# Performance work log

Hardware: AMD Instinct MI355X
Metric: run time of the kernel (lower is better)

Reference implementation:

```python
import jax, jax.numpy as jnp
import numpy as np
from jax import lax

N, M, T, IN, H, DEPTH = 64, 10, 160, 40, 256, 3
B = N * M
EPS = 1e-8


def setup_inputs() -> dict:
    key = jax.random.key(0)
    ks = jax.random.split(key, 20)
    s = 1.0 / np.sqrt(H)  # torch LSTM init scale
    inp = {
        "sequences": jax.random.normal(ks[0], (B, T, IN), jnp.float32),
        "len_sequences": jax.random.randint(ks[1], (B,), 80, T + 1, jnp.int32),
        "w_sim": jnp.float32(0.5),
        "b_sim": jnp.float32(0.5),
    }
    in_sizes = [IN, H, H]
    for l in range(DEPTH):
        k = 2 + 4 * l
        inp[f"Wih{l}"] = jax.random.uniform(ks[k], (4 * H, in_sizes[l]), jnp.float32, -s, s)
        inp[f"Whh{l}"] = jax.random.uniform(ks[k + 1], (4 * H, H), jnp.float32, -s, s)
        inp[f"bih{l}"] = jax.random.uniform(ks[k + 2], (4 * H,), jnp.float32, -s, s)
        inp[f"bhh{l}"] = jax.random.uniform(ks[k + 3], (4 * H,), jnp.float32, -s, s)
    return inp


def _lstm_layer(x_tbf, mask_tb, Wih, Whh, bih, bhh):
    """x_tbf: [T,B,F] time-major. mask_tb: [T,B] valid-step mask.
    Returns (h_seq [T,B,H], c_last [B,H]) where c_last is the cell state at
    the last valid timestep of each sequence (packed-sequence semantics)."""
    b = x_tbf.shape[1]
    h0 = jnp.zeros((b, H), x_tbf.dtype)
    c0 = jnp.zeros((b, H), x_tbf.dtype)

    def step(carry, xm):
        h, c = carry
        xt, mt = xm
        g = xt @ Wih.T + bih + h @ Whh.T + bhh  # [B,4H]
        i, f, gg, o = jnp.split(g, 4, axis=1)
        cn = jax.nn.sigmoid(f) * c + jax.nn.sigmoid(i) * jnp.tanh(gg)
        hn = jax.nn.sigmoid(o) * jnp.tanh(cn)
        m = mt[:, None]
        h2 = jnp.where(m, hn, h)
        c2 = jnp.where(m, cn, c)
        return (h2, c2), h2

    (hT, cT), h_seq = lax.scan(step, (h0, c0), (x_tbf, mask_tb))
    return h_seq, cT


def reference(sequences, len_sequences, Wih0, Whh0, bih0, bhh0,
              Wih1, Whh1, bih1, bhh1, Wih2, Whh2, bih2, bhh2,
              w_sim, b_sim):
    lens = len_sequences.astype(jnp.int32)
    x = jnp.transpose(sequences, (1, 0, 2))  # [T,B,IN]
    mask = jnp.arange(T)[:, None] < lens[None, :]  # [T,B]

    layers = [(Wih0, Whh0, bih0, bhh0), (Wih1, Whh1, bih1, bhh1), (Wih2, Whh2, bih2, bhh2)]
    c_last = None
    for (Wih, Whh, bih, bhh) in layers:
        x, c_last = _lstm_layer(x, mask, Wih, Whh, bih, bhh)
    E = c_last  # [B,H] final-layer cell state per utterance (original order)

    # L2-normalize embeddings (F.normalize, p=2, dim=1)
    E = E / jnp.maximum(jnp.linalg.norm(E, axis=1, keepdims=True), 1e-12)

    Er = E.reshape(N, M, H)
    C = Er.mean(axis=1)  # [N,H] speaker centroids
    # exclusive centroids exactly as source: (M*c_j + E_i)/(M-1)
    Cm = ((M * C[:, None, :] + Er) / (M - 1)).reshape(B, H)

    En = E / jnp.maximum(jnp.linalg.norm(E, axis=1, keepdims=True), EPS)
    Cn = C / jnp.maximum(jnp.linalg.norm(C, axis=1, keepdims=True), EPS)
    Cmn = Cm / jnp.maximum(jnp.linalg.norm(Cm, axis=1, keepdims=True), EPS)

    S = (En @ Cn.T) * w_sim + b_sim  # [B,N]: cos(E_i, c_j)*w + b

    # diagonal block: row i, col i//M uses exclusive centroid
    d = jnp.sum(En * Cmn, axis=1)  # [B]
    rows = jnp.arange(B)
    cols = jnp.repeat(jnp.arange(N), M)
    S = S.at[rows, cols].set(d * w_sim + b_sim)
    return S


if __name__ == "__main__":
    out = reference(**setup_inputs())
    print(out.shape, out.dtype)
```

## Files before the change

kernel.cpp:

```cpp
#include <hip/hip_runtime.h>
#include <cstdint>
#include <cstddef>

typedef __attribute__((ext_vector_type(8))) short short8;
typedef __attribute__((ext_vector_type(4))) float f32x4;
typedef __attribute__((ext_vector_type(4))) unsigned short us4;

#define N_SPK 64
#define M_UTT 10
#define T_SEQ 160
#define IN_F  40
#define H_DIM 256
#define B_TOT 640
#define G4    1024
#define FSTR  64

__device__ __forceinline__ unsigned short f2bf(float f) {
  unsigned int u = __float_as_uint(f);
  u += 0x7FFFu + ((u >> 16) & 1u);
  return (unsigned short)(u >> 16);
}
__device__ __forceinline__ float b2f(unsigned short u) {
  return __uint_as_float(((unsigned int)u) << 16);
}
__device__ __forceinline__ float sigm(float x) {
  return 1.f / (1.f + __expf(-x));
}
__device__ __forceinline__ float tanh_fast(float x) {
  return 1.f - 2.f / (1.f + __expf(2.f * x));
}
__device__ __forceinline__ unsigned long long ato_ld(const unsigned long long* p) {
  return __hip_atomic_load(p, __ATOMIC_RELAXED, __HIP_MEMORY_SCOPE_AGENT);
}
__device__ __forceinline__ void ato_st(unsigned long long* p, unsigned long long v) {
  __hip_atomic_store(p, v, __ATOMIC_RELAXED, __HIP_MEMORY_SCOPE_AGENT);
}
__device__ __forceinline__ int flg_ld(const int* p) {
  return __hip_atomic_load(p, __ATOMIC_RELAXED, __HIP_MEMORY_SCOPE_AGENT);
}
__device__ __forceinline__ void flg_st(int* p, int v) {
  __hip_atomic_store(p, v, __ATOMIC_RELAXED, __HIP_MEMORY_SCOPE_AGENT);
}

__global__ void pack_w_kernel(const float* __restrict__ W, short* __restrict__ out,
                              int Kin, int Ktiles) {
  int idx = blockIdx.x * 256 + threadIdx.x;
  int total = 64 * Ktiles * 64;
  if (idx >= total) return;
  int lane = idx & 63;
  int rest = idx >> 6;
  int ks   = rest % Ktiles;
  int tile = rest / Ktiles;
  int n  = tile * 16 + (lane & 15);
  int k0 = ks * 32 + (lane >> 4) * 8;
  short8 v;
#pragma unroll
  for (int j = 0; j < 8; ++j) {
    int k = k0 + j;
    float f = (k < Kin) ? W[(size_t)n * Kin + k] : 0.f;
    v[j] = (short)f2bf(f);
  }
  *(short8*)&out[(size_t)idx * 8] = v;
}

__global__ void bias_sum_kernel(const float* __restrict__ a, const float* __restrict__ b,
                                float* __restrict__ o) {
  int i = blockIdx.x * 256 + threadIdx.x;
  if (i < G4) o[i] = a[i] + b[i];
}

__global__ __launch_bounds__(256, 2)
void gate_gemm0(const float* __restrict__ seq, const short* __restrict__ Wp,
                const float* __restrict__ bias, unsigned short* __restrict__ G) {
  const int btile = blockIdx.x % 40;
  const int rest  = blockIdx.x / 40;
  const int tg    = rest & 3;
  const int chunk = rest >> 2;
  const int tid = threadIdx.x, lane = tid & 63, wave = tid >> 6;
  const int nl = lane & 15, mq = lane >> 4;

  for (int mg = 0; mg < 4; ++mg) {
    const int t0 = chunk * 16 + mg * 4;
    f32x4 acc[4][4];
#pragma unroll
    for (int q = 0; q < 4; ++q) {
      int tile = tg * 16 + wave + 4 * q;
      float bv = bias[tile * 16 + nl];
#pragma unroll
      for (int mm = 0; mm < 4; ++mm) acc[mm][q] = (f32x4){bv, bv, bv, bv};
    }
    for (int kt = 0; kt < 2; ++kt) {
      short8 a[4];
      const int m = btile * 16 + nl;
      const int k0 = kt * 32 + mq * 8;
#pragma unroll
      for (int mm = 0; mm < 4; ++mm) {
#pragma unroll
        for (int j = 0; j < 8; ++j) {
          int k = k0 + j;
          float f = (k < IN_F) ? seq[((size_t)m * T_SEQ + (t0 + mm)) * IN_F + k] : 0.f;
          a[mm][j] = (short)f2bf(f);
        }
      }
#pragma unroll
      for (int q = 0; q < 4; ++q) {
        int tile = tg * 16 + wave + 4 * q;
        short8 b = *(const short8*)&Wp[(((size_t)tile * 2 + kt) * 64 + lane) * 8];
#pragma unroll
        for (int mm = 0; mm < 4; ++mm)
          acc[mm][q] = __builtin_amdgcn_mfma_f32_16x16x32_bf16(a[mm], b, acc[mm][q], 0, 0, 0);
      }
    }
#pragma unroll
    for (int mm = 0; mm < 4; ++mm)
#pragma unroll
      for (int q = 0; q < 4; ++q) {
        int tile = tg * 16 + wave + 4 * q;
        us4 o;
#pragma unroll
        for (int r = 0; r < 4; ++r) o[r] = f2bf(acc[mm][q][r]);
        *(us4*)&G[(((size_t)(t0 + mm) * 40 + btile) * 64 + tile) * 256 + lane * 4] = o;
      }
  }
}

template<int L>
__device__ __forceinline__ void rec_stage(
    int S, int hb,
    const short* __restrict__ Whhp, const short* __restrict__ Wihp,
    const unsigned short* __restrict__ G0, const float* __restrict__ biasl,
    unsigned long long* __restrict__ hxch, int* __restrict__ flags,
    const int* __restrict__ lens, float* __restrict__ c_state,
    unsigned short* h_sh, unsigned short* x_sh, float* c_sh,
    float* bias_sh, short* wih_lds, int* len_sh)
{
  const int tid = threadIdx.x, lane = tid & 63, wave = tid >> 6;
  const int mq = lane >> 4, nl = lane & 15;
  const int lc = wave * 16 + nl;
  const int colown = hb * 64 + lc;
  unsigned long long* x64 = (unsigned long long*)x_sh;

  short8 wregH[4][8];
#pragma unroll
  for (int g = 0; g < 4; ++g) {
    const int tile = g * 16 + hb * 4 + wave;
#pragma unroll
    for (int kt = 0; kt < 8; ++kt)
      wregH[g][kt] = *(const short8*)&Whhp[(((size_t)tile * 8 + kt) * 64 + lane) * 8];
  }
  short8 wregI[4][4];
  if (L >= 1) {
#pragma unroll
    for (int g = 0; g < 4; ++g) {
      const int tile = g * 16 + hb * 4 + wave;
#pragma unroll
      for (int kt = 0; kt < 4; ++kt)
        wregI[g][kt] = *(const short8*)&Wihp[(((size_t)tile * 8 + kt) * 64 + lane) * 8];
    }
    for (int i = tid; i < 4096; i += 256) {
      int tl = i >> 6, ln = i & 63;
      int lt = tl >> 2, kt4 = tl & 3;
      int gt = (lt >> 2) * 16 + hb * 4 + (lt & 3);
      *(short8*)&wih_lds[(lt * 4 + kt4) * 512 + ln * 8] =
          *(const short8*)&Wihp[(((size_t)gt * 8 + 4 + kt4) * 64 + ln) * 8];
    }
    for (int i = tid; i < 1024; i += 256) bias_sh[i] = biasl[i];
  }
  for (int i = tid; i < 64 * 264; i += 256) h_sh[i] = 0;
  for (int i = tid; i < 64 * 65; i += 256) c_sh[i] = 0.f;
  if (tid < 64) len_sh[tid] = lens[S * 64 + tid];

  if (L == 0) {
    us4 tmp[16];
#pragma unroll
    for (int m = 0; m < 4; ++m)
#pragma unroll
      for (int g = 0; g < 4; ++g) {
        const int tile = g * 16 + hb * 4 + wave;
        tmp[m * 4 + g] = *(const us4*)&G0[(((size_t)0 * 40 + S * 4 + m) * 64 + tile) * 256 + lane * 4];
      }
#pragma unroll
    for (int u = 0; u < 16; ++u)
      x64[u * 256 + tid] = *(unsigned long long*)&tmp[u];
  }
  __syncthreads();

  const int fself = L * 40 + S * 4 + hb;

  for (int t = 0; t < T_SEQ; ++t) {
    const int par = t & 3;
    if (L >= 1 && tid < 4)
      while (flg_ld(&flags[((L - 1) * 40 + S * 4 + tid) * FSTR]) < t + 1) {}
    if (L < 2 && tid >= 4 && tid < 8)
      while (flg_ld(&flags[((L + 1) * 40 + S * 4 + (tid - 4)) * FSTR]) < t - 3) {}
    __syncthreads();

    unsigned long long xr[16];
    if (L >= 1) {
      const unsigned long long* xb =
          hxch + ((size_t)((par * 3 + (L - 1)) * 10 + S)) * 4096;
#pragma unroll
      for (int u = 0; u < 16; ++u) xr[u] = ato_ld(&xb[u * 256 + tid]);
    }
    f32x4 acc[4][4];
    if (L == 0) {
#pragma unroll
      for (int m = 0; m < 4; ++m)
#pragma unroll
        for (int g = 0; g < 4; ++g) {
          unsigned long long v = x64[(m * 4 + g) * 256 + tid];
          us4 gv = *(us4*)&v;
#pragma unroll
          for (int r = 0; r < 4; ++r) acc[m][g][r] = b2f(gv[r]);
        }
    } else {
#pragma unroll
      for (int g = 0; g < 4; ++g) {
        const int tile = g * 16 + hb * 4 + wave;
        float bv = bias_sh[tile * 16 + nl];
#pragma unroll
        for (int m = 0; m < 4; ++m) acc[m][g] = (f32x4){bv, bv, bv, bv};
      }
    }
#pragma unroll
    for (int kt = 0; kt < 8; ++kt) {
      short8 a[4];
#pragma unroll
      for (int m = 0; m < 4; ++m)
        a[m] = *(const short8*)&h_sh[(m * 16 + nl) * 264 + kt * 32 + mq * 8];
#pragma unroll
      for (int m = 0; m < 4; ++m)
#pragma unroll
        for (int g = 0; g < 4; ++g)
          acc[m][g] = __builtin_amdgcn_mfma_f32_16x16x32_bf16(a[m], wregH[g][kt], acc[m][g], 0, 0, 0);
    }
    if (L >= 1) {
#pragma unroll
      for (int u = 0; u < 16; ++u) {
        int j = u * 256 + tid, pp = j >> 10, jj = j & 1023;
        *(unsigned long long*)&x_sh[(jj >> 4) * 264 + pp * 64 + (jj & 15) * 4] = xr[u];
      }
      __syncthreads();
#pragma unroll
      for (int kt = 0; kt < 8; ++kt) {
        short8 a[4];
#pragma unroll
        for (int m = 0; m < 4; ++m)
          a[m] = *(const short8*)&x_sh[(m * 16 + nl) * 264 + kt * 32 + mq * 8];
#pragma unroll
        for (int g = 0; g < 4; ++g) {
          short8 b = (kt < 4) ? wregI[g][kt]
                              : *(const short8*)&wih_lds[((g * 4 + wave) * 4 + (kt - 4)) * 512 + lane * 8];
#pragma unroll
          for (int m = 0; m < 4; ++m)
            acc[m][g] = __builtin_amdgcn_mfma_f32_16x16x32_bf16(a[m], b, acc[m][g], 0, 0, 0);
        }
      }
    }
    unsigned short hv[16];
#pragma unroll
    for (int m = 0; m < 4; ++m)
#pragma unroll
      for (int r = 0; r < 4; ++r) {
        const int row = m * 16 + mq * 4 + r;
        float c_old = c_sh[row * 65 + lc];
        float cn = sigm(acc[m][1][r]) * c_old + sigm(acc[m][0][r]) * tanh_fast(acc[m][2][r]);
        float hn = sigm(acc[m][3][r]) * tanh_fast(cn);
        bool upd = t < len_sh[row];
        if (upd) c_sh[row * 65 + lc] = cn;
        hv[m * 4 + r] = upd ? f2bf(hn) : h_sh[row * 264 + colown];
      }
    __syncthreads();
#pragma unroll
    for (int m = 0; m < 4; ++m)
#pragma unroll
      for (int r = 0; r < 4; ++r)
        h_sh[(m * 16 + mq * 4 + r) * 264 + colown] = hv[m * 4 + r];
    __syncthreads();
    unsigned long long* myslab =
        hxch + ((size_t)((par * 3 + L) * 10 + S) * 4 + hb) * 1024;
    for (int j = tid; j < 1024; j += 256) {
      int sample = j >> 4, l4 = j & 15;
      unsigned long long v =
          *(const unsigned long long*)&h_sh[sample * 264 + hb * 64 + l4 * 4];
      ato_st(&myslab[j], v);
    }
    __syncthreads();
    if (tid == 0) flg_st(&flags[fself * FSTR], t + 1);
    if (L == 0) {
      int tn = (t + 1 < T_SEQ) ? t + 1 : t;
      us4 tmp[16];
#pragma unroll
      for (int m = 0; m < 4; ++m)
#pragma unroll
        for (int g = 0; g < 4; ++g) {
          const int tile = g * 16 + hb * 4 + wave;
          tmp[m * 4 + g] = *(const us4*)&G0[(((size_t)tn * 40 + S * 4 + m) * 64 + tile) * 256 + lane * 4];
        }
#pragma unroll
      for (int u = 0; u < 16; ++u)
        x64[u * 256 + tid] = *(unsigned long long*)&tmp[u];
    }
    if (tid < 3) {
      int p = tid + (tid >= hb ? 1 : 0);
      while (flg_ld(&flags[(L * 40 + S * 4 + p) * FSTR]) < t + 1) {}
    }
    __syncthreads();
    {
      unsigned long long pr[12];
#pragma unroll
      for (int u = 0; u < 12; ++u) {
        int j = u * 256 + tid;
        int pp = j >> 10, jj = j & 1023;
        int p = pp + (pp >= hb ? 1 : 0);
        pr[u] = ato_ld(&hxch[((size_t)((par * 3 + L) * 10 + S) * 4 + p) * 1024 + jj]);
      }
#pragma unroll
      for (int u = 0; u < 12; ++u) {
        int j = u * 256 + tid;
        int pp = j >> 10, jj = j & 1023;
        int p = pp + (pp >= hb ? 1 : 0);
        *(unsigned long long*)&h_sh[(jj >> 4) * 264 + p * 64 + (jj & 15) * 4] = pr[u];
      }
    }
    __syncthreads();
  }
  if (L == 2) {
#pragma unroll
    for (int m = 0; m < 4; ++m)
#pragma unroll
      for (int r = 0; r < 4; ++r) {
        const int row = m * 16 + mq * 4 + r;
        c_state[((size_t)S * 64 + row) * 256 + colown] = c_sh[row * 65 + lc];
      }
  }
}

__global__ __launch_bounds__(256, 1)
void fused_lstm(const short* __restrict__ Whhp_all, const short* __restrict__ Wih1p,
                const short* __restrict__ Wih2p, const float* __restrict__ biasc,
                const unsigned short* __restrict__ G0, const int* __restrict__ lens,
                unsigned long long* __restrict__ hxch, int* __restrict__ flags,
                float* __restrict__ c_state)
{
  __shared__ unsigned short h_sh[64 * 264];
  __shared__ unsigned short x_sh[64 * 264];
  __shared__ float c_sh[64 * 65];
  __shared__ float bias_sh[1024];
  __shared__ short wih_lds[16 * 4 * 512];
  __shared__ int len_sh[64];

  const int bid  = blockIdx.x;
  const int xcd  = bid & 7;
  const int j    = bid >> 3;
  const int g    = (j >> 2) * 8 + xcd;
  if (g >= 30) return;
  const int L  = g / 10;
  const int S  = g % 10;
  const int hb = j & 3;

  if (L == 0)
    rec_stage<0>(S, hb, Whhp_all,          nullptr, G0, nullptr,
                 hxch, flags, lens, c_state, h_sh, x_sh, c_sh, bias_sh, wih_lds, len_sh);
  else if (L == 1)
    rec_stage<1>(S, hb, Whhp_all + 262144, Wih1p, G0, biasc + G4,
                 hxch, flags, lens, c_state, h_sh, x_sh, c_sh, bias_sh, wih_lds, len_sh);
  else
    rec_stage<2>(S, hb, Whhp_all + 524288, Wih2p, G0, biasc + 2 * G4,
                 hxch, flags, lens, c_state, h_sh, x_sh, c_sh, bias_sh, wih_lds, len_sh);
}

__global__ void k_norm(const float* __restrict__ E, float* __restrict__ E1,
                       float* __restrict__ En) {
  int row  = blockIdx.x * 4 + (threadIdx.x >> 6);
  int lane = threadIdx.x & 63;
  const float* e = E + (size_t)row * H_DIM;
  float v[4]; float ss = 0.f;
#pragma unroll
  for (int j = 0; j < 4; ++j) { v[j] = e[lane + 64 * j]; ss += v[j] * v[j]; }
#pragma unroll
  for (int m = 32; m >= 1; m >>= 1) ss += __shfl_xor(ss, m, 64);
  float nrm  = sqrtf(ss);
  float inv1 = 1.f / fmaxf(nrm, 1e-12f);
  float inv2 = 1.f / fmaxf(nrm * inv1, 1e-8f);
#pragma unroll
  for (int j = 0; j < 4; ++j) {
    float e1 = v[j] * inv1;
    E1[(size_t)row * H_DIM + lane + 64 * j] = e1;
    En[(size_t)row * H_DIM + lane + 64 * j] = e1 * inv2;
  }
}

__global__ void k_cent(const float* __restrict__ E1, float* __restrict__ C,
                       float* __restrict__ CnT) {
  int n = blockIdx.x;
  int lane = threadIdx.x;
  float v[4]; float ss = 0.f;
#pragma unroll
  for (int j = 0; j < 4; ++j) {
    int col = lane + 64 * j;
    float s = 0.f;
    for (int m = 0; m < M_UTT; ++m) s += E1[((size_t)n * M_UTT + m) * H_DIM + col];
    v[j] = s / (float)M_UTT;
    ss += v[j] * v[j];
  }
#pragma unroll
  for (int m = 32; m >= 1; m >>= 1) ss += __shfl_xor(ss, m, 64);
  float inv = 1.f / fmaxf(sqrtf(ss), 1e-8f);
#pragma unroll
  for (int j = 0; j < 4; ++j) {
    int col = lane + 64 * j;
    C[(size_t)n * H_DIM + col]  = v[j];
    CnT[(size_t)col * N_SPK + n] = v[j] * inv;
  }
}

__global__ void k_cm(const float* __restrict__ E1, const float* __restrict__ C,
                     float* __restrict__ Cmn) {
  int b    = blockIdx.x * 4 + (threadIdx.x >> 6);
  int lane = threadIdx.x & 63;
  int spk  = b / M_UTT;
  float v[4]; float ss = 0.f;
#pragma unroll
  for (int j = 0; j < 4; ++j) {
    int col = lane + 64 * j;
    v[j] = ((float)M_UTT * C[(size_t)spk * H_DIM + col] + E1[(size_t)b * H_DIM + col])
           / (float)(M_UTT - 1);
    ss += v[j] * v[j];
  }
#pragma unroll
  for (int m = 32; m >= 1; m >>= 1) ss += __shfl_xor(ss, m, 64);
  float inv = 1.f / fmaxf(sqrtf(ss), 1e-8f);
#pragma unroll
  for (int j = 0; j < 4; ++j)
    Cmn[(size_t)b * H_DIM + lane + 64 * j] = v[j] * inv;
}

__global__ void k_sim(const float* __restrict__ En, const float* __restrict__ CnT,
                      const float* __restrict__ Cmn, const float* __restrict__ w_sim,
                      const float* __restrict__ b_sim, float* __restrict__ S) {
  int b = blockIdx.x;
  int n = threadIdx.x;
  int diag = b / M_UTT;
  float w = w_sim[0], bb = b_sim[0];
  float s = 0.f;
  for (int k = 0; k < H_DIM; ++k) {
    float en = En[(size_t)b * H_DIM + k];
    float c  = (n == diag) ? Cmn[(size_t)b * H_DIM + k] : CnT[(size_t)k * N_SPK + n];
    s += en * c;
  }
  S[(size_t)b * N_SPK + n] = s * w + bb;
}

#define O_WHH   0ull
#define O_WIH0  1572864ull
#define O_WIH1  1703936ull
#define O_WIH2  2228224ull
#define O_BIAS  2752512ull
#define O_CST   2764800ull
#define O_E1    3420160ull
#define O_EN    4075520ull
#define O_C     4730880ull
#define O_CNT   4796416ull
#define O_CMN   4861952ull
#define O_FLG   5517312ull
#define O_HXCH  5548032ull
#define O_G0    9480192ull

extern "C" void kernel_launch(void* const* d_in, const int* in_sizes, int n_in,
                              void* d_out, int out_size, void* d_ws, size_t ws_size,
                              hipStream_t stream) {
  const float* seq   = (const float*)d_in[0];
  const int*   lens  = (const int*)d_in[1];
  const float* w_sim = (const float*)d_in[2];
  const float* b_sim = (const float*)d_in[3];
  const float* Wih[3] = {(const float*)d_in[4],  (const float*)d_in[8],  (const float*)d_in[12]};
  const float* Whh[3] = {(const float*)d_in[5],  (const float*)d_in[9],  (const float*)d_in[13]};
  const float* bih[3] = {(const float*)d_in[6],  (const float*)d_in[10], (const float*)d_in[14]};
  const float* bhh[3] = {(const float*)d_in[7],  (const float*)d_in[11], (const float*)d_in[15]};

  char* ws = (char*)d_ws;
  short* Whhp_all = (short*)(ws + O_WHH);
  short* Wihp[3] = {(short*)(ws + O_WIH0), (short*)(ws + O_WIH1), (short*)(ws + O_WIH2)};
  float* biasc = (float*)(ws + O_BIAS);
  float* c_state = (float*)(ws + O_CST);
  float* E1  = (float*)(ws + O_E1);
  float* En  = (float*)(ws + O_EN);
  float* C   = (float*)(ws + O_C);
  float* CnT = (float*)(ws + O_CNT);
  float* Cmn = (float*)(ws + O_CMN);
  int* flags = (int*)(ws + O_FLG);
  unsigned long long* hxch = (unsigned long long*)(ws + O_HXCH);
  unsigned short* G0 = (unsigned short*)(ws + O_G0);
  float* S = (float*)d_out;

  pack_w_kernel<<<32, 256, 0, stream>>>(Wih[0], Wihp[0], IN_F, 2);
  pack_w_kernel<<<128, 256, 0, stream>>>(Whh[0], Whhp_all, H_DIM, 8);
  pack_w_kernel<<<128, 256, 0, stream>>>(Whh[1], Whhp_all + 262144, H_DIM, 8);
  pack_w_kernel<<<128, 256, 0, stream>>>(Whh[2], Whhp_all + 524288, H_DIM, 8);
  pack_w_kernel<<<128, 256, 0, stream>>>(Wih[1], Wihp[1], H_DIM, 8);
  pack_w_kernel<<<128, 256, 0, stream>>>(Wih[2], Wihp[2], H_DIM, 8);
  for (int l = 0; l < 3; ++l)
    bias_sum_kernel<<<4, 256, 0, stream>>>(bih[l], bhh[l], biasc + l * G4);

  gate_gemm0<<<1600, 256, 0, stream>>>(seq, Wihp[0], biasc, G0);

  hipMemsetAsync(ws + O_FLG, 0, 30720, stream);
  fused_lstm<<<128, 256, 0, stream>>>(Whhp_all, Wihp[1], Wihp[2], biasc, G0, lens,
                                      hxch, flags, c_state);

  k_norm<<<160, 256, 0, stream>>>(c_state, E1, En);
  k_cent<<<N_SPK, 64, 0, stream>>>(E1, C, CnT);
  k_cm<<<160, 256, 0, stream>>>(E1, C, Cmn);
  k_sim<<<B_TOT, 64, 0, stream>>>(En, CnT, Cmn, w_sim, b_sim, S);
}
```

Measured before the change: 1.701 ms.

## Use per-wave flags, keep cell state in registers, and drop block barriers

Cross-block synchronisation in the recurrent LSTM loop moves from one flag per block to one flag per wave. Each wave publishes its own slice of h and sets its own flag after a vmcnt wait, and each wave spins on all producer flags itself, so several block-wide __syncthreads can be dropped. The cell state moves from LDS into per-thread registers, and the flag stride shrinks to fit four times as many flags. The aim is to cut barrier and flag latency on the serial time-step critical path, at the cost of more flag polling traffic and subtler ordering that relies on each wave reading only the LDS columns it wrote itself.

```diff
diff --git a/kernel.cpp b/kernel.cpp
--- a/kernel.cpp
+++ b/kernel.cpp
@@ -13,7 +13,7 @@
 #define H_DIM 256
 #define B_TOT 640
 #define G4    1024
-#define FSTR  64
+#define FSTR  16
 
 __device__ __forceinline__ unsigned short f2bf(float f) {
   unsigned int u = __float_as_uint(f);
@@ -131,7 +131,7 @@
     const unsigned short* __restrict__ G0, const float* __restrict__ biasl,
     unsigned long long* __restrict__ hxch, int* __restrict__ flags,
     const int* __restrict__ lens, float* __restrict__ c_state,
-    unsigned short* h_sh, unsigned short* x_sh, float* c_sh,
+    unsigned short* h_sh, unsigned short* x_sh,
     float* bias_sh, short* wih_lds, int* len_sh)
 {
   const int tid = threadIdx.x, lane = tid & 63, wave = tid >> 6;
@@ -167,8 +167,11 @@
     for (int i = tid; i < 1024; i += 256) bias_sh[i] = biasl[i];
   }
   for (int i = tid; i < 64 * 264; i += 256) h_sh[i] = 0;
-  for (int i = tid; i < 64 * 65; i += 256) c_sh[i] = 0.f;
   if (tid < 64) len_sh[tid] = lens[S * 64 + tid];
+
+  float creg[16];
+#pragma unroll
+  for (int i = 0; i < 16; ++i) creg[i] = 0.f;
 
   if (L == 0) {
     us4 tmp[16];
@@ -185,15 +188,23 @@
   }
   __syncthreads();
 
-  const int fself = L * 40 + S * 4 + hb;
+  const int fbase = (L * 40 + S * 4 + hb) * 4;
 
   for (int t = 0; t < T_SEQ; ++t) {
     const int par = t & 3;
-    if (L >= 1 && tid < 4)
-      while (flg_ld(&flags[((L - 1) * 40 + S * 4 + tid) * FSTR]) < t + 1) {}
-    if (L < 2 && tid >= 4 && tid < 8)
-      while (flg_ld(&flags[((L + 1) * 40 + S * 4 + (tid - 4)) * FSTR]) < t - 3) {}
-    __syncthreads();
+
+    {
+      const bool doU = (L >= 1) && (lane < 16);
+      const bool doD = (L < 2) && (lane >= 16) && (lane < 32);
+      if (doU || doD) {
+        int ln  = doU ? lane : (lane - 16);
+        int blk = doU ? ((L - 1) * 40 + S * 4 + (ln >> 2))
+                      : ((L + 1) * 40 + S * 4 + (ln >> 2));
+        int thr = doU ? (t + 1) : (t - 3);
+        const int* fp = &flags[(blk * 4 + (ln & 3)) * FSTR];
+        while (flg_ld(fp) < thr) {}
+      }
+    }
 
     unsigned long long xr[16];
     if (L >= 1) {
@@ -257,36 +268,57 @@
         }
       }
     }
-    unsigned short hv[16];
-#pragma unroll
-    for (int m = 0; m < 4; ++m)
-#pragma unroll
-      for (int r = 0; r < 4; ++r) {
-        const int row = m * 16 + mq * 4 + r;
-        float c_old = c_sh[row * 65 + lc];
-        float cn = sigm(acc[m][1][r]) * c_old + sigm(acc[m][0][r]) * tanh_fast(acc[m][2][r]);
-        float hn = sigm(acc[m][3][r]) * tanh_fast(cn);
-        bool upd = t < len_sh[row];
-        if (upd) c_sh[row * 65 + lc] = cn;
-        hv[m * 4 + r] = upd ? f2bf(hn) : h_sh[row * 264 + colown];
-      }
-    __syncthreads();
-#pragma unroll
-    for (int m = 0; m < 4; ++m)
-#pragma unroll
-      for (int r = 0; r < 4; ++r)
-        h_sh[(m * 16 + mq * 4 + r) * 264 + colown] = hv[m * 4 + r];
-    __syncthreads();
+    if (L == 0) {
+      unsigned short hv[16];
+      bool updv[16];
+#pragma unroll
+      for (int m = 0; m < 4; ++m)
+#pragma unroll
+        for (int r = 0; r < 4; ++r) {
+          const int row = m * 16 + mq * 4 + r;
+          float c_old = creg[m * 4 + r];
+          float cn = sigm(acc[m][1][r]) * c_old + sigm(acc[m][0][r]) * tanh_fast(acc[m][2][r]);
+          float hn = sigm(acc[m][3][r]) * tanh_fast(cn);
+          bool upd = t < len_sh[row];
+          if (upd) creg[m * 4 + r] = cn;
+          hv[m * 4 + r] = f2bf(hn);
+          updv[m * 4 + r] = upd;
+        }
+      __syncthreads();
+#pragma unroll
+      for (int m = 0; m < 4; ++m)
+#pragma unroll
+        for (int r = 0; r < 4; ++r)
+          if (updv[m * 4 + r])
+            h_sh[(m * 16 + mq * 4 + r) * 264 + colown] = hv[m * 4 + r];
+    } else {
+#pragma unroll
+      for (int m = 0; m < 4; ++m)
+#pragma unroll
+        for (int r = 0; r < 4; ++r) {
+          const int row = m * 16 + mq * 4 + r;
+          float c_old = creg[m * 4 + r];
+          float cn = sigm(acc[m][1][r]) * c_old + sigm(acc[m][0][r]) * tanh_fast(acc[m][2][r]);
+          float hn = sigm(acc[m][3][r]) * tanh_fast(cn);
+          if (t < len_sh[row]) {
+            creg[m * 4 + r] = cn;
+            h_sh[row * 264 + colown] = f2bf(hn);
+          }
+        }
+    }
     unsigned long long* myslab =
         hxch + ((size_t)((par * 3 + L) * 10 + S) * 4 + hb) * 1024;
-    for (int j = tid; j < 1024; j += 256) {
-      int sample = j >> 4, l4 = j & 15;
-      unsigned long long v =
-          *(const unsigned long long*)&h_sh[sample * 264 + hb * 64 + l4 * 4];
-      ato_st(&myslab[j], v);
-    }
-    __syncthreads();
-    if (tid == 0) flg_st(&flags[fself * FSTR], t + 1);
+    {
+      unsigned long long pv[4];
+#pragma unroll
+      for (int q = 0; q < 4; ++q)
+        pv[q] = *(const unsigned long long*)&h_sh[lane * 264 + hb * 64 + (wave * 4 + q) * 4];
+#pragma unroll
+      for (int q = 0; q < 4; ++q)
+        ato_st(&myslab[lane * 16 + wave * 4 + q], pv[q]);
+      asm volatile("s_waitcnt vmcnt(0)" ::: "memory");
+      if (lane == 0) flg_st(&flags[(fbase + wave) * FSTR], t + 1);
+    }
     if (L == 0) {
       int tn = (t + 1 < T_SEQ) ? t + 1 : t;
       us4 tmp[16];
@@ -301,11 +333,12 @@
       for (int u = 0; u < 16; ++u)
         x64[u * 256 + tid] = *(unsigned long long*)&tmp[u];
     }
-    if (tid < 3) {
-      int p = tid + (tid >= hb ? 1 : 0);
-      while (flg_ld(&flags[(L * 40 + S * 4 + p) * FSTR]) < t + 1) {}
-    }
-    __syncthreads();
+    if (lane < 12) {
+      int p = lane >> 2;
+      p += (p >= hb) ? 1 : 0;
+      const int* fp = &flags[((L * 40 + S * 4 + p) * 4 + (lane & 3)) * FSTR];
+      while (flg_ld(fp) < t + 1) {}
+    }
     {
       unsigned long long pr[12];
 #pragma unroll
@@ -331,7 +364,7 @@
 #pragma unroll
       for (int r = 0; r < 4; ++r) {
         const int row = m * 16 + mq * 4 + r;
-        c_state[((size_t)S * 64 + row) * 256 + colown] = c_sh[row * 65 + lc];
+        c_state[((size_t)S * 64 + row) * 256 + colown] = creg[m * 4 + r];
       }
   }
 }
@@ -345,7 +378,6 @@
 {
   __shared__ unsigned short h_sh[64 * 264];
   __shared__ unsigned short x_sh[64 * 264];
-  __shared__ float c_sh[64 * 65];
   __shared__ float bias_sh[1024];
   __shared__ short wih_lds[16 * 4 * 512];
   __shared__ int len_sh[64];
@@ -361,13 +393,13 @@
 
   if (L == 0)
     rec_stage<0>(S, hb, Whhp_all,          nullptr, G0, nullptr,
-                 hxch, flags, lens, c_state, h_sh, x_sh, c_sh, bias_sh, wih_lds, len_sh);
+                 hxch, flags, lens, c_state, h_sh, x_sh, bias_sh, wih_lds, len_sh);
   else if (L == 1)
     rec_stage<1>(S, hb, Whhp_all + 262144, Wih1p, G0, biasc + G4,
-                 hxch, flags, lens, c_state, h_sh, x_sh, c_sh, bias_sh, wih_lds, len_sh);
+                 hxch, flags, lens, c_state, h_sh, x_sh, bias_sh, wih_lds, len_sh);
   else
     rec_stage<2>(S, hb, Whhp_all + 524288, Wih2p, G0, biasc + 2 * G4,
-                 hxch, flags, lens, c_state, h_sh, x_sh, c_sh, bias_sh, wih_lds, len_sh);
+                 hxch, flags, lens, c_state, h_sh, x_sh, bias_sh, wih_lds, len_sh);
 }
 
 __global__ void k_norm(const float* __restrict__ E, float* __restrict__ E1,
```

Result: slower. 1.940 ms (+14.1%).

## Replace flag polling with tagged data words in the LSTM hidden-state exchange

Applied to the files above, without the earlier changes.

Each 32-bit hidden-state word exchanged between blocks is now packed with a timestep tag in a 64-bit atomic store. Consumers poll on the tags directly instead of waiting on separate per-block flags and extra barriers. The recurrent MFMA loop is rotated so each block first works on its own hidden-state slice while peer slices are in flight, and layer-input loads are issued before the remaining MFMAs. The cell state moves from LDS into registers and the G0 prefetch stays in registers. In exchange the exchange buffer doubles in size, must be zeroed by a larger memset, and uses three-way instead of four-way buffering, which costs more memory traffic and register pressure.

```diff
diff --git a/kernel.cpp b/kernel.cpp
--- a/kernel.cpp
+++ b/kernel.cpp
@@ -131,22 +131,23 @@
     const unsigned short* __restrict__ G0, const float* __restrict__ biasl,
     unsigned long long* __restrict__ hxch, int* __restrict__ flags,
     const int* __restrict__ lens, float* __restrict__ c_state,
-    unsigned short* h_sh, unsigned short* x_sh, float* c_sh,
+    unsigned short* h_sh, unsigned short* x_sh,
     float* bias_sh, short* wih_lds, int* len_sh)
 {
   const int tid = threadIdx.x, lane = tid & 63, wave = tid >> 6;
   const int mq = lane >> 4, nl = lane & 15;
   const int lc = wave * 16 + nl;
   const int colown = hb * 64 + lc;
-  unsigned long long* x64 = (unsigned long long*)x_sh;
 
   short8 wregH[4][8];
 #pragma unroll
   for (int g = 0; g < 4; ++g) {
     const int tile = g * 16 + hb * 4 + wave;
 #pragma unroll
-    for (int kt = 0; kt < 8; ++kt)
-      wregH[g][kt] = *(const short8*)&Whhp[(((size_t)tile * 8 + kt) * 64 + lane) * 8];
+    for (int s = 0; s < 8; ++s) {
+      const int ktp = (2 * hb + s) & 7;
+      wregH[g][s] = *(const short8*)&Whhp[(((size_t)tile * 8 + ktp) * 64 + lane) * 8];
+    }
   }
   short8 wregI[4][4];
   if (L >= 1) {
@@ -167,52 +168,39 @@
     for (int i = tid; i < 1024; i += 256) bias_sh[i] = biasl[i];
   }
   for (int i = tid; i < 64 * 264; i += 256) h_sh[i] = 0;
-  for (int i = tid; i < 64 * 65; i += 256) c_sh[i] = 0.f;
   if (tid < 64) len_sh[tid] = lens[S * 64 + tid];
 
+  float creg[16];
+#pragma unroll
+  for (int i = 0; i < 16; ++i) creg[i] = 0.f;
+
+  us4 g0reg[16];
   if (L == 0) {
-    us4 tmp[16];
 #pragma unroll
     for (int m = 0; m < 4; ++m)
 #pragma unroll
       for (int g = 0; g < 4; ++g) {
         const int tile = g * 16 + hb * 4 + wave;
-        tmp[m * 4 + g] = *(const us4*)&G0[(((size_t)0 * 40 + S * 4 + m) * 64 + tile) * 256 + lane * 4];
-      }
-#pragma unroll
-    for (int u = 0; u < 16; ++u)
-      x64[u * 256 + tid] = *(unsigned long long*)&tmp[u];
+        g0reg[m * 4 + g] =
+            *(const us4*)&G0[(((size_t)0 * 40 + S * 4 + m) * 64 + tile) * 256 + lane * 4];
+      }
   }
   __syncthreads();
 
   const int fself = L * 40 + S * 4 + hb;
+  unsigned long long pr[24];
 
   for (int t = 0; t < T_SEQ; ++t) {
-    const int par = t & 3;
-    if (L >= 1 && tid < 4)
-      while (flg_ld(&flags[((L - 1) * 40 + S * 4 + tid) * FSTR]) < t + 1) {}
-    if (L < 2 && tid >= 4 && tid < 8)
-      while (flg_ld(&flags[((L + 1) * 40 + S * 4 + (tid - 4)) * FSTR]) < t - 3) {}
-    __syncthreads();
-
-    unsigned long long xr[16];
-    if (L >= 1) {
-      const unsigned long long* xb =
-          hxch + ((size_t)((par * 3 + (L - 1)) * 10 + S)) * 4096;
-#pragma unroll
-      for (int u = 0; u < 16; ++u) xr[u] = ato_ld(&xb[u * 256 + tid]);
-    }
+    const int par = t % 3;
+
     f32x4 acc[4][4];
     if (L == 0) {
 #pragma unroll
       for (int m = 0; m < 4; ++m)
 #pragma unroll
-        for (int g = 0; g < 4; ++g) {
-          unsigned long long v = x64[(m * 4 + g) * 256 + tid];
-          us4 gv = *(us4*)&v;
-#pragma unroll
-          for (int r = 0; r < 4; ++r) acc[m][g][r] = b2f(gv[r]);
-        }
+        for (int g = 0; g < 4; ++g)
+#pragma unroll
+          for (int r = 0; r < 4; ++r) acc[m][g][r] = b2f(g0reg[m * 4 + g][r]);
     } else {
 #pragma unroll
       for (int g = 0; g < 4; ++g) {
@@ -223,24 +211,91 @@
       }
     }
 #pragma unroll
-    for (int kt = 0; kt < 8; ++kt) {
+    for (int s = 0; s < 2; ++s) {
+      const int ktp = (2 * hb + s) & 7;
       short8 a[4];
 #pragma unroll
       for (int m = 0; m < 4; ++m)
-        a[m] = *(const short8*)&h_sh[(m * 16 + nl) * 264 + kt * 32 + mq * 8];
+        a[m] = *(const short8*)&h_sh[(m * 16 + nl) * 264 + ktp * 32 + mq * 8];
 #pragma unroll
       for (int m = 0; m < 4; ++m)
 #pragma unroll
         for (int g = 0; g < 4; ++g)
-          acc[m][g] = __builtin_amdgcn_mfma_f32_16x16x32_bf16(a[m], wregH[g][kt], acc[m][g], 0, 0, 0);
-    }
+          acc[m][g] = __builtin_amdgcn_mfma_f32_16x16x32_bf16(a[m], wregH[g][s], acc[m][g], 0, 0, 0);
+    }
+    if (t > 0) {
+      const int parv = (t + 2) % 3;
+      const unsigned long long* grpv =
+          hxch + (size_t)((parv * 3 + L) * 10 + S) * 8192;
+      const int expv = t;
+      bool redo = true;
+      while (redo) {
+        redo = false;
+#pragma unroll
+        for (int u = 0; u < 24; ++u) {
+          if ((int)(pr[u] >> 32) < expv) {
+            int glob = u * 256 + tid;
+            int pp = glob >> 11, g = glob & 2047;
+            int p = pp + (pp >= hb ? 1 : 0);
+            pr[u] = ato_ld(&grpv[p * 2048 + g]);
+            redo = true;
+          }
+        }
+      }
+#pragma unroll
+      for (int u = 0; u < 24; ++u) {
+        int glob = u * 256 + tid;
+        int pp = glob >> 11, g = glob & 2047;
+        int p = pp + (pp >= hb ? 1 : 0);
+        int j = g >> 1, half = g & 1;
+        *(unsigned int*)&h_sh[(j >> 4) * 264 + p * 64 + (j & 15) * 4 + half * 2] =
+            (unsigned int)pr[u];
+      }
+    }
+    __syncthreads();
+
+    unsigned long long xr[32];
+    const unsigned long long* xb = nullptr;
     if (L >= 1) {
-#pragma unroll
-      for (int u = 0; u < 16; ++u) {
-        int j = u * 256 + tid, pp = j >> 10, jj = j & 1023;
-        *(unsigned long long*)&x_sh[(jj >> 4) * 264 + pp * 64 + (jj & 15) * 4] = xr[u];
+      xb = hxch + (size_t)((par * 3 + (L - 1)) * 10 + S) * 8192;
+#pragma unroll
+      for (int u = 0; u < 32; ++u) xr[u] = ato_ld(&xb[u * 256 + tid]);
+    }
+#pragma unroll
+    for (int s = 2; s < 8; ++s) {
+      const int ktp = (2 * hb + s) & 7;
+      short8 a[4];
+#pragma unroll
+      for (int m = 0; m < 4; ++m)
+        a[m] = *(const short8*)&h_sh[(m * 16 + nl) * 264 + ktp * 32 + mq * 8];
+#pragma unroll
+      for (int m = 0; m < 4; ++m)
+#pragma unroll
+        for (int g = 0; g < 4; ++g)
+          acc[m][g] = __builtin_amdgcn_mfma_f32_16x16x32_bf16(a[m], wregH[g][s], acc[m][g], 0, 0, 0);
+    }
+    if (L >= 1) {
+      const int expx = t + 1;
+      bool redo = true;
+      while (redo) {
+        redo = false;
+#pragma unroll
+        for (int u = 0; u < 32; ++u)
+          if ((int)(xr[u] >> 32) < expx) {
+            xr[u] = ato_ld(&xb[u * 256 + tid]);
+            redo = true;
+          }
+      }
+#pragma unroll
+      for (int u = 0; u < 32; ++u) {
+        int glob = u * 256 + tid;
+        int pp = glob >> 11, g = glob & 2047;
+        int j = g >> 1, half = g & 1;
+        *(unsigned int*)&x_sh[(j >> 4) * 264 + pp * 64 + (j & 15) * 4 + half * 2] =
+            (unsigned int)xr[u];
       }
       __syncthreads();
+      if (tid == 0) flg_st(&flags[fself * FSTR], t + 1);
 #pragma unroll
       for (int kt = 0; kt < 8; ++kt) {
         short8 a[4];
@@ -263,11 +318,11 @@
 #pragma unroll
       for (int r = 0; r < 4; ++r) {
         const int row = m * 16 + mq * 4 + r;
-        float c_old = c_sh[row * 65 + lc];
+        float c_old = creg[m * 4 + r];
         float cn = sigm(acc[m][1][r]) * c_old + sigm(acc[m][0][r]) * tanh_fast(acc[m][2][r]);
         float hn = sigm(acc[m][3][r]) * tanh_fast(cn);
         bool upd = t < len_sh[row];
-        if (upd) c_sh[row * 65 + lc] = cn;
+        if (upd) creg[m * 4 + r] = cn;
         hv[m * 4 + r] = upd ? f2bf(hn) : h_sh[row * 264 + colown];
       }
     __syncthreads();
@@ -276,54 +331,42 @@
 #pragma unroll
       for (int r = 0; r < 4; ++r)
         h_sh[(m * 16 + mq * 4 + r) * 264 + colown] = hv[m * 4 + r];
+    if (L < 2 && tid >= 4 && tid < 8)
+      while (flg_ld(&flags[((L + 1) * 40 + S * 4 + (tid - 4)) * FSTR]) < t - 2) {}
     __syncthreads();
     unsigned long long* myslab =
-        hxch + ((size_t)((par * 3 + L) * 10 + S) * 4 + hb) * 1024;
-    for (int j = tid; j < 1024; j += 256) {
-      int sample = j >> 4, l4 = j & 15;
-      unsigned long long v =
-          *(const unsigned long long*)&h_sh[sample * 264 + hb * 64 + l4 * 4];
-      ato_st(&myslab[j], v);
-    }
-    __syncthreads();
-    if (tid == 0) flg_st(&flags[fself * FSTR], t + 1);
+        hxch + ((size_t)((par * 3 + L) * 10 + S) * 4 + hb) * 2048;
+    const unsigned long long tagw = ((unsigned long long)(unsigned)(t + 1)) << 32;
+#pragma unroll
+    for (int i = 0; i < 8; ++i) {
+      int g = i * 256 + tid;
+      int j = g >> 1, half = g & 1;
+      unsigned int d =
+          *(const unsigned int*)&h_sh[(j >> 4) * 264 + hb * 64 + (j & 15) * 4 + half * 2];
+      ato_st(&myslab[g], tagw | (unsigned long long)d);
+    }
     if (L == 0) {
       int tn = (t + 1 < T_SEQ) ? t + 1 : t;
-      us4 tmp[16];
 #pragma unroll
       for (int m = 0; m < 4; ++m)
 #pragma unroll
         for (int g = 0; g < 4; ++g) {
           const int tile = g * 16 + hb * 4 + wave;
-          tmp[m * 4 + g] = *(const us4*)&G0[(((size_t)tn * 40 + S * 4 + m) * 64 + tile) * 256 + lane * 4];
+          g0reg[m * 4 + g] =
+              *(const us4*)&G0[(((size_t)tn * 40 + S * 4 + m) * 64 + tile) * 256 + lane * 4];
         }
-#pragma unroll
-      for (int u = 0; u < 16; ++u)
-        x64[u * 256 + tid] = *(unsigned long long*)&tmp[u];
-    }
-    if (tid < 3) {
-      int p = tid + (tid >= hb ? 1 : 0);
-      while (flg_ld(&flags[(L * 40 + S * 4 + p) * FSTR]) < t + 1) {}
-    }
-    __syncthreads();
+    }
     {
-      unsigned long long pr[12];
-#pragma unroll
-      for (int u = 0; u < 12; ++u) {
-        int j = u * 256 + tid;
-        int pp = j >> 10, jj = j & 1023;
+      const unsigned long long* grp =
+          hxch + (size_t)((par * 3 + L) * 10 + S) * 8192;
+#pragma unroll
+      for (int u = 0; u < 24; ++u) {
+        int glob = u * 256 + tid;
+        int pp = glob >> 11, g = glob & 2047;
         int p = pp + (pp >= hb ? 1 : 0);
-        pr[u] = ato_ld(&hxch[((size_t)((par * 3 + L) * 10 + S) * 4 + p) * 1024 + jj]);
-      }
-#pragma unroll
-      for (int u = 0; u < 12; ++u) {
-        int j = u * 256 + tid;
-        int pp = j >> 10, jj = j & 1023;
-        int p = pp + (pp >= hb ? 1 : 0);
-        *(unsigned long long*)&h_sh[(jj >> 4) * 264 + p * 64 + (jj & 15) * 4] = pr[u];
-      }
-    }
-    __syncthreads();
+        pr[u] = ato_ld(&grp[p * 2048 + g]);
+      }
+    }
   }
   if (L == 2) {
 #pragma unroll
@@ -331,7 +374,7 @@
 #pragma unroll
       for (int r = 0; r < 4; ++r) {
         const int row = m * 16 + mq * 4 + r;
-        c_state[((size_t)S * 64 + row) * 256 + colown] = c_sh[row * 65 + lc];
+        c_state[((size_t)S * 64 + row) * 256 + colown] = creg[m * 4 + r];
       }
   }
 }
@@ -345,7 +388,6 @@
 {
   __shared__ unsigned short h_sh[64 * 264];
   __shared__ unsigned short x_sh[64 * 264];
-  __shared__ float c_sh[64 * 65];
   __shared__ float bias_sh[1024];
   __shared__ short wih_lds[16 * 4 * 512];
   __shared__ int len_sh[64];
@@ -361,13 +403,13 @@
 
   if (L == 0)
     rec_stage<0>(S, hb, Whhp_all,          nullptr, G0, nullptr,
-                 hxch, flags, lens, c_state, h_sh, x_sh, c_sh, bias_sh, wih_lds, len_sh);
+                 hxch, flags, lens, c_state, h_sh, x_sh, bias_sh, wih_lds, len_sh);
   else if (L == 1)
     rec_stage<1>(S, hb, Whhp_all + 262144, Wih1p, G0, biasc + G4,
-                 hxch, flags, lens, c_state, h_sh, x_sh, c_sh, bias_sh, wih_lds, len_sh);
+                 hxch, flags, lens, c_state, h_sh, x_sh, bias_sh, wih_lds, len_sh);
   else
     rec_stage<2>(S, hb, Whhp_all + 524288, Wih2p, G0, biasc + 2 * G4,
-                 hxch, flags, lens, c_state, h_sh, x_sh, c_sh, bias_sh, wih_lds, len_sh);
+                 hxch, flags, lens, c_state, h_sh, x_sh, bias_sh, wih_lds, len_sh);
 }
 
 __global__ void k_norm(const float* __restrict__ E, float* __restrict__ E1,
@@ -458,14 +500,14 @@
 #define O_WIH2  2228224ull
 #define O_BIAS  2752512ull
 #define O_CST   2764800ull
-#define O_E1    3420160ull
-#define O_EN    4075520ull
-#define O_C     4730880ull
-#define O_CNT   4796416ull
-#define O_CMN   4861952ull
-#define O_FLG   5517312ull
-#define O_HXCH  5548032ull
-#define O_G0    9480192ull
+#define O_FLG   3420160ull
+#define O_HXCH  3450880ull
+#define O_E1    (O_HXCH)
+#define O_EN    (O_HXCH + 655360ull)
+#define O_C     (O_HXCH + 1310720ull)
+#define O_CNT   (O_HXCH + 1376256ull)
+#define O_CMN   (O_HXCH + 1441792ull)
+#define O_G0    9349120ull
 
 extern "C" void kernel_launch(void* const* d_in, const int* in_sizes, int n_in,
                               void* d_out, int out_size, void* d_ws, size_t ws_size,
@@ -505,7 +547,7 @@
 
   gate_gemm0<<<1600, 256, 0, stream>>>(seq, Wihp[0], biasc, G0);
 
-  hipMemsetAsync(ws + O_FLG, 0, 30720, stream);
+  hipMemsetAsync(ws + O_FLG, 0, 30720 + 5898240, stream);
   fused_lstm<<<128, 256, 0, stream>>>(Whhp_all, Wihp[1], Wihp[2], biasc, G0, lens,
                                       hxch, flags, c_state);
 
```

Measured after the change: 2.502 ms. +47.1%, slower.

## Prefetch next-step layer input during h exchange and keep cell state in registers

Applied to the files above, without the earlier changes.

Moves the wait on the previous layer's flag and the global load of its next-timestep hidden output into the end-of-step exchange phase. That fetch now overlaps the peer h-slab reads, and the x tile is ready at the start of the next step. The per-block cell state moves from an LDS array into 16 registers per thread, and the final-step exchange is skipped. It adds register pressure (16 more xr values live across the loop) and changes the inter-layer synchronisation ordering, which risks stalls or correctness bugs if the flag logic is wrong.

```diff
diff --git a/kernel.cpp b/kernel.cpp
--- a/kernel.cpp
+++ b/kernel.cpp
@@ -131,7 +131,7 @@
     const unsigned short* __restrict__ G0, const float* __restrict__ biasl,
     unsigned long long* __restrict__ hxch, int* __restrict__ flags,
     const int* __restrict__ lens, float* __restrict__ c_state,
-    unsigned short* h_sh, unsigned short* x_sh, float* c_sh,
+    unsigned short* h_sh, unsigned short* x_sh,
     float* bias_sh, short* wih_lds, int* len_sh)
 {
   const int tid = threadIdx.x, lane = tid & 63, wave = tid >> 6;
@@ -167,8 +167,11 @@
     for (int i = tid; i < 1024; i += 256) bias_sh[i] = biasl[i];
   }
   for (int i = tid; i < 64 * 264; i += 256) h_sh[i] = 0;
-  for (int i = tid; i < 64 * 65; i += 256) c_sh[i] = 0.f;
   if (tid < 64) len_sh[tid] = lens[S * 64 + tid];
+
+  float creg[16];
+#pragma unroll
+  for (int i = 0; i < 16; ++i) creg[i] = 0.f;
 
   if (L == 0) {
     us4 tmp[16];
@@ -187,20 +190,30 @@
 
   const int fself = L * 40 + S * 4 + hb;
 
+  unsigned long long xr[16];
+  if (L >= 1) {
+    if (tid < 4)
+      while (flg_ld(&flags[((L - 1) * 40 + S * 4 + tid) * FSTR]) < 1) {}
+    __syncthreads();
+    const unsigned long long* xb0 =
+        hxch + ((size_t)((0 * 3 + (L - 1)) * 10 + S)) * 4096;
+#pragma unroll
+    for (int u = 0; u < 16; ++u) xr[u] = ato_ld(&xb0[u * 256 + tid]);
+  }
+
   for (int t = 0; t < T_SEQ; ++t) {
     const int par = t & 3;
-    if (L >= 1 && tid < 4)
-      while (flg_ld(&flags[((L - 1) * 40 + S * 4 + tid) * FSTR]) < t + 1) {}
-    if (L < 2 && tid >= 4 && tid < 8)
-      while (flg_ld(&flags[((L + 1) * 40 + S * 4 + (tid - 4)) * FSTR]) < t - 3) {}
-    __syncthreads();
-
-    unsigned long long xr[16];
+
+    if (L < 2 && tid < 4)
+      while (flg_ld(&flags[((L + 1) * 40 + S * 4 + tid) * FSTR]) < t - 3) {}
+
     if (L >= 1) {
-      const unsigned long long* xb =
-          hxch + ((size_t)((par * 3 + (L - 1)) * 10 + S)) * 4096;
-#pragma unroll
-      for (int u = 0; u < 16; ++u) xr[u] = ato_ld(&xb[u * 256 + tid]);
+#pragma unroll
+      for (int u = 0; u < 16; ++u) {
+        int j = u * 256 + tid, pp = j >> 10, jj = j & 1023;
+        *(unsigned long long*)&x_sh[(jj >> 4) * 264 + pp * 64 + (jj & 15) * 4] = xr[u];
+      }
+      __syncthreads();
     }
     f32x4 acc[4][4];
     if (L == 0) {
@@ -236,12 +249,6 @@
     }
     if (L >= 1) {
 #pragma unroll
-      for (int u = 0; u < 16; ++u) {
-        int j = u * 256 + tid, pp = j >> 10, jj = j & 1023;
-        *(unsigned long long*)&x_sh[(jj >> 4) * 264 + pp * 64 + (jj & 15) * 4] = xr[u];
-      }
-      __syncthreads();
-#pragma unroll
       for (int kt = 0; kt < 8; ++kt) {
         short8 a[4];
 #pragma unroll
@@ -263,11 +270,11 @@
 #pragma unroll
       for (int r = 0; r < 4; ++r) {
         const int row = m * 16 + mq * 4 + r;
-        float c_old = c_sh[row * 65 + lc];
+        float c_old = creg[m * 4 + r];
         float cn = sigm(acc[m][1][r]) * c_old + sigm(acc[m][0][r]) * tanh_fast(acc[m][2][r]);
         float hn = sigm(acc[m][3][r]) * tanh_fast(cn);
         bool upd = t < len_sh[row];
-        if (upd) c_sh[row * 65 + lc] = cn;
+        if (upd) creg[m * 4 + r] = cn;
         hv[m * 4 + r] = upd ? f2bf(hn) : h_sh[row * 264 + colown];
       }
     __syncthreads();
@@ -301,29 +308,39 @@
       for (int u = 0; u < 16; ++u)
         x64[u * 256 + tid] = *(unsigned long long*)&tmp[u];
     }
-    if (tid < 3) {
-      int p = tid + (tid >= hb ? 1 : 0);
-      while (flg_ld(&flags[(L * 40 + S * 4 + p) * FSTR]) < t + 1) {}
-    }
-    __syncthreads();
-    {
-      unsigned long long pr[12];
-#pragma unroll
-      for (int u = 0; u < 12; ++u) {
-        int j = u * 256 + tid;
-        int pp = j >> 10, jj = j & 1023;
-        int p = pp + (pp >= hb ? 1 : 0);
-        pr[u] = ato_ld(&hxch[((size_t)((par * 3 + L) * 10 + S) * 4 + p) * 1024 + jj]);
-      }
-#pragma unroll
-      for (int u = 0; u < 12; ++u) {
-        int j = u * 256 + tid;
-        int pp = j >> 10, jj = j & 1023;
-        int p = pp + (pp >= hb ? 1 : 0);
-        *(unsigned long long*)&h_sh[(jj >> 4) * 264 + p * 64 + (jj & 15) * 4] = pr[u];
-      }
-    }
-    __syncthreads();
+    if (t + 1 < T_SEQ) {
+      if (tid < 3) {
+        int p = tid + (tid >= hb ? 1 : 0);
+        while (flg_ld(&flags[(L * 40 + S * 4 + p) * FSTR]) < t + 1) {}
+      }
+      if (L >= 1 && tid >= 64 && tid < 68)
+        while (flg_ld(&flags[((L - 1) * 40 + S * 4 + (tid - 64)) * FSTR]) < t + 2) {}
+      __syncthreads();
+      if (L >= 1) {
+        const unsigned long long* xb =
+            hxch + ((size_t)((((t + 1) & 3) * 3 + (L - 1)) * 10 + S)) * 4096;
+#pragma unroll
+        for (int u = 0; u < 16; ++u) xr[u] = ato_ld(&xb[u * 256 + tid]);
+      }
+      {
+        unsigned long long pr[12];
+#pragma unroll
+        for (int u = 0; u < 12; ++u) {
+          int j = u * 256 + tid;
+          int pp = j >> 10, jj = j & 1023;
+          int p = pp + (pp >= hb ? 1 : 0);
+          pr[u] = ato_ld(&hxch[((size_t)((par * 3 + L) * 10 + S) * 4 + p) * 1024 + jj]);
+        }
+#pragma unroll
+        for (int u = 0; u < 12; ++u) {
+          int j = u * 256 + tid;
+          int pp = j >> 10, jj = j & 1023;
+          int p = pp + (pp >= hb ? 1 : 0);
+          *(unsigned long long*)&h_sh[(jj >> 4) * 264 + p * 64 + (jj & 15) * 4] = pr[u];
+        }
+      }
+      __syncthreads();
+    }
   }
   if (L == 2) {
 #pragma unroll
@@ -331,7 +348,7 @@
 #pragma unroll
       for (int r = 0; r < 4; ++r) {
         const int row = m * 16 + mq * 4 + r;
-        c_state[((size_t)S * 64 + row) * 256 + colown] = c_sh[row * 65 + lc];
+        c_state[((size_t)S * 64 + row) * 256 + colown] = creg[m * 4 + r];
       }
   }
 }
@@ -345,7 +362,6 @@
 {
   __shared__ unsigned short h_sh[64 * 264];
   __shared__ unsigned short x_sh[64 * 264];
-  __shared__ float c_sh[64 * 65];
   __shared__ float bias_sh[1024];
   __shared__ short wih_lds[16 * 4 * 512];
   __shared__ int len_sh[64];
@@ -361,13 +377,13 @@
 
   if (L == 0)
     rec_stage<0>(S, hb, Whhp_all,          nullptr, G0, nullptr,
-                 hxch, flags, lens, c_state, h_sh, x_sh, c_sh, bias_sh, wih_lds, len_sh);
+                 hxch, flags, lens, c_state, h_sh, x_sh, bias_sh, wih_lds, len_sh);
   else if (L == 1)
     rec_stage<1>(S, hb, Whhp_all + 262144, Wih1p, G0, biasc + G4,
-                 hxch, flags, lens, c_state, h_sh, x_sh, c_sh, bias_sh, wih_lds, len_sh);
+                 hxch, flags, lens, c_state, h_sh, x_sh, bias_sh, wih_lds, len_sh);
   else
     rec_stage<2>(S, hb, Whhp_all + 524288, Wih2p, G0, biasc + 2 * G4,
-                 hxch, flags, lens, c_state, h_sh, x_sh, c_sh, bias_sh, wih_lds, len_sh);
+                 hxch, flags, lens, c_state, h_sh, x_sh, bias_sh, wih_lds, len_sh);
 }
 
 __global__ void k_norm(const float* __restrict__ E, float* __restrict__ E1,
```

Result: faster. 1.560 ms (-8.3%).
